# Kernel optimization log

Hardware: AMD Instinct MI355X
Metric: run time of the kernel (lower is better)

## Reference

```python
import jax, jax.numpy as jnp
import numpy as np

N = 100_000      # nodes (single heterogeneous node type)
E = 1_600_000    # edges per relation (avg in-degree ~16)
D = 128          # in_feats
H = 128          # rep_dim
R = 3            # relations


def setup_inputs() -> dict:
    key = jax.random.key(0)
    ks = jax.random.split(key, 1 + 6 * R)
    inp = {"x": jax.random.normal(ks[0], (N, D), jnp.float32)}
    for r in range(R):
        k = ks[1 + 6 * r: 1 + 6 * (r + 1)]
        inp[f"src{r}"] = jax.random.randint(k[0], (E,), 0, N)
        inp[f"dst{r}"] = jax.random.randint(k[1], (E,), 0, N)
        inp[f"w{r}"] = jax.random.uniform(k[2], (E,), jnp.float32)
        inp[f"Wself{r}"] = jax.random.normal(k[3], (D, H), jnp.float32) * 0.05
        inp[f"Wneigh{r}"] = jax.random.normal(k[4], (D, H), jnp.float32) * 0.05
        inp[f"b{r}"] = jax.random.normal(k[5], (H,), jnp.float32) * 0.05
    return inp


def _sage_mean(x, src, dst, w, Wself, Wneigh, b):
    """DGL SAGEConv, aggregator='mean', edge_weight=w, activation=ReLU.

    h_N[v] = (sum_{e:(u->v)} w_e * x[u]) / max(in_deg(v), 1)
    out    = relu(x @ Wself + h_N @ Wneigh + b)
    """
    msg = x[src] * w[:, None]                                   # [E, D] gather
    s = jax.ops.segment_sum(msg, dst, num_segments=N)           # [N, D] scatter-add
    deg = jax.ops.segment_sum(jnp.ones_like(w), dst, num_segments=N)  # [N]
    h_neigh = s / jnp.maximum(deg, 1.0)[:, None]                # mean; 0 for isolated nodes
    return jax.nn.relu(x @ Wself + h_neigh @ Wneigh + b)


def reference(x,
              src0, dst0, w0,
              src1, dst1, w1,
              src2, dst2, w2,
              Wself0, Wneigh0, b0,
              Wself1, Wneigh1, b1,
              Wself2, Wneigh2, b2):
    # HeteroGraphConv(aggregate='mean'): average the per-relation SAGEConv outputs.
    o0 = _sage_mean(x, src0, dst0, w0, Wself0, Wneigh0, b0)
    o1 = _sage_mean(x, src1, dst1, w1, Wself1, Wneigh1, b1)
    o2 = _sage_mean(x, src2, dst2, w2, Wself2, Wneigh2, b2)
    return (o0 + o1 + o2) / 3.0
```

## Files before the change

kernel.cpp:

```cpp
#include <hip/hip_runtime.h>
#include <hip/hip_bf16.h>
#include <cstdio>
#include <cstdint>
#include <cstddef>

#define NN 100000
#define EE 1600000
#define DD 128

#define BKT 196
#define RSHIFT 9
#define RANGE 512
#define CAP 9500
#define EPB 2048
#define ABLK ((EE + EPB - 1) / EPB)

typedef __attribute__((ext_vector_type(8))) short short8;
typedef __attribute__((ext_vector_type(4))) float floatx4;

__device__ __forceinline__ float bf2f(unsigned short u) {
    union { unsigned int u; float f; } c;
    c.u = ((unsigned int)u) << 16;
    return c.f;
}
__device__ __forceinline__ float hi2f(unsigned int p) {
    union { unsigned int u; float f; } c;
    c.u = p & 0xffff0000u;
    return c.f;
}
__device__ __forceinline__ float lo2f(unsigned int p) {
    union { unsigned int u; float f; } c;
    c.u = p << 16;
    return c.f;
}
__device__ __forceinline__ unsigned short f2bf(float f) {
    union { float f; unsigned int u; } c;
    c.f = f;
    unsigned int lsb = (c.u >> 16) & 1u;
    c.u += 0x7fffu + lsb;
    return (unsigned short)(c.u >> 16);
}

__global__ void detect_kernel(const void* x, const void* w, const void* Wm,
                              const void* b, int* flags) {
    __shared__ int ok_s;
    int bid = blockIdx.x, tid = threadIdx.x;
    if (tid == 0) ok_s = 0;
    __syncthreads();
    const unsigned short* p;
    int n;
    if (bid == 0)      { p = (const unsigned short*)x;  n = 1024; }
    else if (bid == 1) { p = (const unsigned short*)w;  n = 1024; }
    else if (bid == 2) { p = (const unsigned short*)Wm; n = 1024; }
    else               { p = (const unsigned short*)b;  n = 128;  }
    int ok = 0;
    for (int i = tid; i < n; i += blockDim.x) {
        unsigned short u = p[i];
        int e = (u >> 7) & 0xff;
        if (u == 0 || u == 0x8000 || (e >= 90 && e <= 127)) ok++;
    }
    atomicAdd(&ok_s, ok);
    __syncthreads();
    if (tid == 0) flags[bid] = (ok_s * 4 >= n * 3) ? 1 : 0;
}

__global__ void conv_x_kernel(const void* src, unsigned short* dst, int n4,
                              const int* flag) {
    if (*flag) return;
    int i = blockIdx.x * blockDim.x + threadIdx.x;
    if (i >= n4) return;
    float4 f = ((const float4*)src)[i];
    uint2 o;
    o.x = (unsigned int)f2bf(f.x) | ((unsigned int)f2bf(f.y) << 16);
    o.y = (unsigned int)f2bf(f.z) | ((unsigned int)f2bf(f.w) << 16);
    ((uint2*)dst)[i] = o;
}

__global__ void conv_bias_kernel(const void* b0, const void* b1,
                                 const void* b2, float* dst,
                                 const int* flag) {
    int r = blockIdx.x;
    const void* src = (r == 0) ? b0 : (r == 1) ? b1 : b2;
    int i = threadIdx.x;
    if (i >= DD) return;
    if (*flag) dst[r * DD + i] = bf2f(((const unsigned short*)src)[i]);
    else       dst[r * DD + i] = ((const float*)src)[i];
}

__global__ void wfrag_kernel(const void* W0s, const void* W0n, const void* W1s,
                             const void* W1n, const void* W2s, const void* W2n,
                             unsigned short* out, const int* flag) {
    int mat = blockIdx.x >> 3;
    const void* W = (mat == 0) ? W0s : (mat == 1) ? W0n : (mat == 2) ? W1s
                  : (mat == 3) ? W1n : (mat == 4) ? W2s : W2n;
    int gid = (blockIdx.x & 7) * 256 + threadIdx.x;
    int nt = gid >> 8;
    int kc = (gid >> 6) & 3;
    int lane = gid & 63;
    int n = nt * 16 + (lane & 15);
    int k0 = kc * 32 + (lane >> 4) * 8;
    unsigned short v[8];
    if (*flag) {
        const unsigned short* Ws = (const unsigned short*)W;
#pragma unroll
        for (int j = 0; j < 8; j++) v[j] = Ws[(k0 + j) * DD + n];
    } else {
        const float* Ws = (const float*)W;
#pragma unroll
        for (int j = 0; j < 8; j++) v[j] = f2bf(Ws[(k0 + j) * DD + n]);
    }
    *(short8*)(out + (size_t)mat * DD * DD + (size_t)gid * 8) = *(short8*)v;
}

__global__ void __launch_bounds__(256) countA_kernel(
    const int* __restrict__ d0, const int* __restrict__ d1,
    const int* __restrict__ d2, int* __restrict__ cnts) {
    __shared__ int hist[BKT];
    const int rel = blockIdx.x / ABLK;
    const int blk = blockIdx.x - rel * ABLK;
    const int* dstp = (rel == 0) ? d0 : (rel == 1) ? d1 : d2;
    int* cn = cnts + (size_t)rel * ABLK * BKT;
    const int tid = threadIdx.x;
    const int base = blk * EPB;
    for (int i = tid; i < BKT; i += 256) hist[i] = 0;
    __syncthreads();
#pragma unroll
    for (int k = 0; k < 8; k++) {
        int i = base + k * 256 + tid;
        if (i < EE) atomicAdd(&hist[dstp[i] >> RSHIFT], 1);
    }
    __syncthreads();
    for (int i = tid; i < BKT; i += 256)
        cn[(size_t)blk * BKT + i] = hist[i];
}

__global__ void __launch_bounds__(256) scanA_kernel(
    const int* __restrict__ cnts, int* __restrict__ bases,
    int* __restrict__ gcur) {
    __shared__ int s[256];
    const int rel = blockIdx.x / BKT;
    const int b = blockIdx.x - rel * BKT;
    const int* cn = cnts + (size_t)rel * ABLK * BKT;
    int* bs = bases + (size_t)rel * ABLK * BKT;
    const int tid = threadIdx.x;
    const int per = (ABLK + 255) / 256;
    int v[4];
    int sum = 0;
#pragma unroll
    for (int k = 0; k < 4; k++) {
        int idx = tid * per + k;
        v[k] = (idx < ABLK) ? cn[(size_t)idx * BKT + b] : 0;
        sum += v[k];
    }
    s[tid] = sum;
    __syncthreads();
    for (int o = 1; o < 256; o <<= 1) {
        int t = (tid >= o) ? s[tid - o] : 0;
        __syncthreads();
        s[tid] += t;
        __syncthreads();
    }
    int running = s[tid] - sum;
#pragma unroll
    for (int k = 0; k < 4; k++) {
        int idx = tid * per + k;
        if (idx < ABLK) bs[(size_t)idx * BKT + b] = running;
        running += v[k];
    }
    if (tid == 255) gcur[rel * BKT + b] = s[255];
}

__global__ void __launch_bounds__(256) placeA_kernel(
    const int* __restrict__ srcp, const int* __restrict__ dstp,
    const void* __restrict__ wp, const int* __restrict__ bases,
    int2* __restrict__ ebin, const int* __restrict__ wflag) {
    __shared__ int hist[BKT];
    __shared__ int off[BKT];
    __shared__ int cur[BKT];
    __shared__ int gbase[BKT];
    __shared__ int scan[256];
    __shared__ int2 sorted[EPB];
    __shared__ unsigned char slotb[EPB];
    const int tid = threadIdx.x;
    const int base = blockIdx.x * EPB;
    for (int i = tid; i < BKT; i += 256) hist[i] = 0;
    __syncthreads();
    int myd[8];
#pragma unroll
    for (int k = 0; k < 8; k++) {
        int i = base + k * 256 + tid;
        int d = (i < EE) ? dstp[i] : -1;
        myd[k] = d;
        if (d >= 0) atomicAdd(&hist[d >> RSHIFT], 1);
    }
    __syncthreads();
    int hv = (tid < BKT) ? hist[tid] : 0;
    scan[tid] = hv;
    __syncthreads();
    for (int o = 1; o < 256; o <<= 1) {
        int v = (tid >= o) ? scan[tid - o] : 0;
        __syncthreads();
        scan[tid] += v;
        __syncthreads();
    }
    if (tid < BKT) {
        off[tid] = scan[tid] - hv;
        cur[tid] = scan[tid] - hv;
        gbase[tid] = bases[(size_t)blockIdx.x * BKT + tid];
    }
    __syncthreads();
    const bool wbf = (*wflag != 0);
#pragma unroll
    for (int k = 0; k < 8; k++) {
        int d = myd[k];
        if (d < 0) continue;
        int i = base + k * 256 + tid;
        int b = d >> RSHIFT;
        int dloc = d - (b << RSHIFT);
        int s = srcp[i];
        float wv = wbf ? bf2f(((const unsigned short*)wp)[i])
                       : ((const float*)wp)[i];
        union { float f; int i; } c; c.f = wv;
        int pos = atomicAdd(&cur[b], 1);
        sorted[pos] = make_int2(s | (dloc << 17), c.i);
        slotb[pos] = (unsigned char)b;
    }
    __syncthreads();
    const int total = min(EPB, EE - base);
    for (int i = tid; i < total; i += 256) {
        int b = slotb[i];
        int g = gbase[b] + (i - off[b]);
        if (g < CAP) ebin[(size_t)b * CAP + g] = sorted[i];
    }
}

__global__ void __launch_bounds__(256) bucketsort_kernel(
    const int2* __restrict__ ebin, const int* __restrict__ gcur,
    int2* __restrict__ es2, int2* __restrict__ ptrv) {
    __shared__ int hc[RANGE];
    __shared__ int off[RANGE];
    __shared__ int scan[256];
    const int b = blockIdx.x, tid = threadIdx.x;
    const int base = b * CAP;
    const int cnt = min(gcur[b], CAP);
    for (int i = tid; i < RANGE; i += 256) hc[i] = 0;
    __syncthreads();
    for (int i = tid; i < cnt; i += 256) {
        int dl = ebin[base + i].x >> 17;
        atomicAdd(&hc[dl], 1);
    }
    __syncthreads();
    int a0 = hc[2 * tid], a1 = hc[2 * tid + 1];
    scan[tid] = a0 + a1;
    __syncthreads();
    for (int o = 1; o < 256; o <<= 1) {
        int v = (tid >= o) ? scan[tid - o] : 0;
        __syncthreads();
        scan[tid] += v;
        __syncthreads();
    }
    int ex = scan[tid] - (a0 + a1);
    off[2 * tid] = ex;
    off[2 * tid + 1] = ex + a0;
    ptrv[b * RANGE + 2 * tid]     = make_int2(base + ex, a0);
    ptrv[b * RANGE + 2 * tid + 1] = make_int2(base + ex + a0, a1);
    __syncthreads();
    hc[2 * tid] = off[2 * tid];
    hc[2 * tid + 1] = off[2 * tid + 1];
    __syncthreads();
    for (int i = tid; i < cnt; i += 256) {
        int2 rec = ebin[base + i];
        int dl = rec.x >> 17;
        int p = atomicAdd(&hc[dl], 1);
        es2[base + p] = make_int2(rec.x & 0x1FFFF, rec.y);
    }
}

__global__ void __launch_bounds__(256) aggregate_kernel(
    const int2* __restrict__ es2, const int2* __restrict__ ptrv,
    const unsigned short* __restrict__ xc, const void* __restrict__ xraw,
    const int* __restrict__ xflag, unsigned short* __restrict__ hout) {
    int gw = (blockIdx.x * blockDim.x + threadIdx.x) >> 6;
    int lane = threadIdx.x & 63;
    if (gw >= 3 * NN) return;
    int rel = gw / NN;
    int node = gw - rel * NN;
    const unsigned int* x32 = (*xflag) ? (const unsigned int*)xraw
                                       : (const unsigned int*)xc;
    const int2* es = es2 + (size_t)rel * BKT * CAP;
    int2 pc = ptrv[(size_t)rel * BKT * RANGE + node];
    int beg = pc.x, deg = pc.y, end = beg + deg;
    float a0 = 0.f, a1 = 0.f;
    int e = beg;
    for (; e + 16 <= end; e += 16) {
        unsigned int p[16];
        float cw[16];
#pragma unroll
        for (int k = 0; k < 16; k++) {
            int2 r = es[e + k];
            p[k] = x32[(size_t)r.x * 64 + lane];
            union { int i; float f; } c; c.i = r.y;
            cw[k] = c.f;
        }
#pragma unroll
        for (int k = 0; k < 16; k++) {
            a0 += cw[k] * lo2f(p[k]);
            a1 += cw[k] * hi2f(p[k]);
        }
    }
    for (; e + 4 <= end; e += 4) {
        int2 r0 = es[e], r1 = es[e + 1], r2 = es[e + 2], r3 = es[e + 3];
        unsigned int p0 = x32[(size_t)r0.x * 64 + lane];
        unsigned int p1 = x32[(size_t)r1.x * 64 + lane];
        unsigned int p2 = x32[(size_t)r2.x * 64 + lane];
        unsigned int p3 = x32[(size_t)r3.x * 64 + lane];
        union { int i; float f; } c0, c1, c2, c3;
        c0.i = r0.y; c1.i = r1.y; c2.i = r2.y; c3.i = r3.y;
        a0 += c0.f * lo2f(p0); a1 += c0.f * hi2f(p0);
        a0 += c1.f * lo2f(p1); a1 += c1.f * hi2f(p1);
        a0 += c2.f * lo2f(p2); a1 += c2.f * hi2f(p2);
        a0 += c3.f * lo2f(p3); a1 += c3.f * hi2f(p3);
    }
    for (; e < end; e++) {
        int2 r0 = es[e];
        unsigned int p0 = x32[(size_t)r0.x * 64 + lane];
        union { int i; float f; } c0; c0.i = r0.y;
        a0 += c0.f * lo2f(p0); a1 += c0.f * hi2f(p0);
    }
    float inv = 1.0f / (float)(deg > 1 ? deg : 1);
    unsigned int outv = ((unsigned int)f2bf(a1 * inv) << 16) | f2bf(a0 * inv);
    ((unsigned int*)hout)[(size_t)gw * 64 + lane] = outv;
}

__global__ void __launch_bounds__(256) output_kernel(
    const unsigned short* __restrict__ xc, const void* __restrict__ xraw,
    const unsigned short* __restrict__ h, const unsigned short* __restrict__ wf,
    const float* __restrict__ bc, void* out, const int* __restrict__ flag) {
    __shared__ unsigned short lds[DD * DD];
    const int tid = threadIdx.x;
    const int wv = tid >> 6, lane = tid & 63;
    const int tile = blockIdx.x * 4 + wv;
    const bool active = tile < (NN / 16);
    const int c = lane & 15, q = lane >> 4;
    const int nodeRow = tile * 16 + c;
    const int xbf = *flag;
    const unsigned short* xs = xbf ? (const unsigned short*)xraw : xc;

    short8 xfrag[4];
    if (active) {
#pragma unroll
        for (int kc = 0; kc < 4; kc++)
            xfrag[kc] = *(const short8*)(xs + (size_t)nodeRow * DD + kc * 32 +
                                         q * 8);
    }

    floatx4 outacc[8];
#pragma unroll
    for (int i = 0; i < 8; i++) outacc[i] = (floatx4){0.f, 0.f, 0.f, 0.f};

    for (int r = 0; r < 3; r++) {
        floatx4 acc[8];
#pragma unroll
        for (int i = 0; i < 8; i++) acc[i] = (floatx4){0.f, 0.f, 0.f, 0.f};
        for (int p = 0; p < 2; p++) {
            __syncthreads();
            {
                const int4* src = (const int4*)(wf + (size_t)(r * 2 + p) * DD * DD);
                int4* dst = (int4*)lds;
#pragma unroll
                for (int it = 0; it < 8; it++)
                    dst[tid + it * 256] = src[tid + it * 256];
            }
            __syncthreads();
            if (active) {
#pragma unroll
                for (int kc = 0; kc < 4; kc++) {
                    short8 afrag;
                    if (p == 0) {
                        afrag = xfrag[kc];
                    } else {
                        afrag = *(const short8*)(h + (size_t)r * NN * DD +
                                                 (size_t)nodeRow * DD +
                                                 kc * 32 + q * 8);
                    }
#pragma unroll
                    for (int nt = 0; nt < 8; nt++) {
                        short8 bfrag = *(const short8*)(
                            &lds[((nt * 4 + kc) * 64 + lane) * 8]);
                        acc[nt] = __builtin_amdgcn_mfma_f32_16x16x32_bf16(
                            afrag, bfrag, acc[nt], 0, 0, 0);
                    }
                }
            }
        }
        if (active) {
#pragma unroll
            for (int nt = 0; nt < 8; nt++) {
                float bv = bc[r * DD + nt * 16 + c];
#pragma unroll
                for (int i = 0; i < 4; i++) {
                    float v = acc[nt][i] + bv;
                    outacc[nt][i] += fmaxf(v, 0.f);
                }
            }
        }
    }
    if (active) {
        const float sc = 1.f / 3.f;
        if (xbf) {
            unsigned short* o = (unsigned short*)out;
#pragma unroll
            for (int nt = 0; nt < 8; nt++)
#pragma unroll
                for (int i = 0; i < 4; i++)
                    o[(size_t)(tile * 16 + q * 4 + i) * DD + nt * 16 + c] =
                        f2bf(outacc[nt][i] * sc);
        } else {
            float* o = (float*)out;
#pragma unroll
            for (int nt = 0; nt < 8; nt++)
#pragma unroll
                for (int i = 0; i < 4; i++)
                    o[(size_t)(tile * 16 + q * 4 + i) * DD + nt * 16 + c] =
                        outacc[nt][i] * sc;
        }
    }
}

extern "C" void kernel_launch(void* const* d_in, const int* in_sizes, int n_in,
                              void* d_out, int out_size, void* d_ws,
                              size_t ws_size, hipStream_t stream) {
    char* w = (char*)d_ws;
    size_t off = 0;
    auto alloc = [&](size_t bytes) {
        size_t o = off;
        off = (off + bytes + 255) & ~(size_t)255;
        return o;
    };
    size_t o_flags = alloc(4 * sizeof(int));
    size_t o_gcur  = alloc(3 * BKT * sizeof(int));
    size_t o_bc    = alloc(3 * DD * sizeof(float));
    size_t o_wf    = alloc(6 * DD * DD * sizeof(unsigned short));
    size_t o_xc    = alloc((size_t)NN * DD * sizeof(unsigned short));
    size_t o_cnts  = alloc((size_t)3 * ABLK * BKT * sizeof(int));
    size_t o_bases = alloc((size_t)3 * ABLK * BKT * sizeof(int));
    size_t o_ebin  = alloc((size_t)BKT * CAP * sizeof(int2));
    size_t o_es2   = alloc((size_t)3 * BKT * CAP * sizeof(int2));
    size_t o_ptrv  = alloc((size_t)3 * BKT * RANGE * sizeof(int2));
    size_t o_h     = alloc((size_t)3 * NN * DD * sizeof(unsigned short));
    if (ws_size < off) {
        fprintf(stderr, "kernel_launch: ws_size=%zu < needed=%zu\n", ws_size,
                off);
        return;
    }
    int* flags          = (int*)(w + o_flags);
    int* gcur           = (int*)(w + o_gcur);
    float* bc           = (float*)(w + o_bc);
    unsigned short* wf  = (unsigned short*)(w + o_wf);
    unsigned short* xc  = (unsigned short*)(w + o_xc);
    int* cnts           = (int*)(w + o_cnts);
    int* bases          = (int*)(w + o_bases);
    int2* ebin          = (int2*)(w + o_ebin);
    int2* es2           = (int2*)(w + o_es2);
    int2* ptrv          = (int2*)(w + o_ptrv);
    unsigned short* hh  = (unsigned short*)(w + o_h);

    const void* x_in = d_in[0];

    detect_kernel<<<4, 256, 0, stream>>>(x_in, d_in[3], d_in[4], d_in[6],
                                         flags);
    conv_x_kernel<<<(NN * DD / 4 + 255) / 256, 256, 0, stream>>>(
        x_in, xc, NN * DD / 4, flags + 0);
    wfrag_kernel<<<48, 256, 0, stream>>>(d_in[4], d_in[5], d_in[10], d_in[11],
                                         d_in[16], d_in[17], wf, flags + 2);
    conv_bias_kernel<<<3, 128, 0, stream>>>(d_in[6], d_in[12], d_in[18], bc,
                                            flags + 3);

    countA_kernel<<<3 * ABLK, 256, 0, stream>>>(
        (const int*)d_in[2], (const int*)d_in[8], (const int*)d_in[14], cnts);
    scanA_kernel<<<3 * BKT, 256, 0, stream>>>(cnts, bases, gcur);

    for (int r = 0; r < 3; r++) {
        int base = 1 + 6 * r;
        placeA_kernel<<<ABLK, 256, 0, stream>>>(
            (const int*)d_in[base + 0], (const int*)d_in[base + 1],
            d_in[base + 2], bases + (size_t)r * ABLK * BKT, ebin, flags + 1);
        bucketsort_kernel<<<BKT, 256, 0, stream>>>(
            ebin, gcur + r * BKT, es2 + (size_t)r * BKT * CAP,
            ptrv + (size_t)r * BKT * RANGE);
    }

    aggregate_kernel<<<(3 * NN + 3) / 4, 256, 0, stream>>>(
        es2, ptrv, xc, x_in, flags + 0, hh);

    const int NTILES = NN / 16;
    output_kernel<<<(NTILES + 3) / 4, 256, 0, stream>>>(xc, x_in, hh, wf, bc,
                                                        d_out, flags + 0);
}
```

Measured before the change: 554.8 us.

## Batch per-relation bucket sort launches and gather two edges per wave in aggregation

The placement and bucket-sort kernels now process all three relations in one launch each, using a separate bin buffer per relation when the workspace is large enough, and fall back to the per-relation loop otherwise. This removes launch serialisation and lets the GPU fill with three times as many blocks. The aggregation kernel now has each half-wave gather a different edge's row with 8-byte loads, combines the halves with a cross-lane shuffle, and makes edge bounds wave-uniform through readfirstlane. This doubles the number of rows fetched in flight per wave, at the cost of extra workspace and a reduction step.

```diff
diff --git a/kernel.cpp b/kernel.cpp
--- a/kernel.cpp
+++ b/kernel.cpp
@@ -32,6 +32,9 @@
     union { unsigned int u; float f; } c;
     c.u = p << 16;
     return c.f;
+}
+__device__ __forceinline__ float i2f(int i) {
+    union { int i; float f; } c; c.i = i; return c.f;
 }
 __device__ __forceinline__ unsigned short f2bf(float f) {
     union { float f; unsigned int u; } c;
@@ -119,7 +122,6 @@
     const int rel = blockIdx.x / ABLK;
     const int blk = blockIdx.x - rel * ABLK;
     const int* dstp = (rel == 0) ? d0 : (rel == 1) ? d1 : d2;
-    int* cn = cnts + (size_t)rel * ABLK * BKT;
     const int tid = threadIdx.x;
     const int base = blk * EPB;
     for (int i = tid; i < BKT; i += 256) hist[i] = 0;
@@ -131,7 +133,7 @@
     }
     __syncthreads();
     for (int i = tid; i < BKT; i += 256)
-        cn[(size_t)blk * BKT + i] = hist[i];
+        cnts[(size_t)blockIdx.x * BKT + i] = hist[i];
 }
 
 __global__ void __launch_bounds__(256) scanA_kernel(
@@ -171,8 +173,11 @@
 }
 
 __global__ void __launch_bounds__(256) placeA_kernel(
-    const int* __restrict__ srcp, const int* __restrict__ dstp,
-    const void* __restrict__ wp, const int* __restrict__ bases,
+    const int* __restrict__ s0, const int* __restrict__ d0,
+    const void* __restrict__ w0, const int* __restrict__ s1,
+    const int* __restrict__ d1, const void* __restrict__ w1,
+    const int* __restrict__ s2, const int* __restrict__ d2,
+    const void* __restrict__ w2, const int* __restrict__ bases,
     int2* __restrict__ ebin, const int* __restrict__ wflag) {
     __shared__ int hist[BKT];
     __shared__ int off[BKT];
@@ -181,8 +186,14 @@
     __shared__ int scan[256];
     __shared__ int2 sorted[EPB];
     __shared__ unsigned char slotb[EPB];
+    const int rel = blockIdx.x / ABLK;
+    const int blk = blockIdx.x - rel * ABLK;
+    const int* srcp = (rel == 0) ? s0 : (rel == 1) ? s1 : s2;
+    const int* dstp = (rel == 0) ? d0 : (rel == 1) ? d1 : d2;
+    const void* wp  = (rel == 0) ? w0 : (rel == 1) ? w1 : w2;
+    int2* eb = ebin + (size_t)rel * BKT * CAP;
     const int tid = threadIdx.x;
-    const int base = blockIdx.x * EPB;
+    const int base = blk * EPB;
     for (int i = tid; i < BKT; i += 256) hist[i] = 0;
     __syncthreads();
     int myd[8];
@@ -230,7 +241,7 @@
     for (int i = tid; i < total; i += 256) {
         int b = slotb[i];
         int g = gbase[b] + (i - off[b]);
-        if (g < CAP) ebin[(size_t)b * CAP + g] = sorted[i];
+        if (g < CAP) eb[(size_t)b * CAP + g] = sorted[i];
     }
 }
 
@@ -240,13 +251,18 @@
     __shared__ int hc[RANGE];
     __shared__ int off[RANGE];
     __shared__ int scan[256];
-    const int b = blockIdx.x, tid = threadIdx.x;
+    const int rel = blockIdx.x / BKT;
+    const int b = blockIdx.x - rel * BKT;
+    const int2* eb = ebin + (size_t)rel * BKT * CAP;
+    int2* es = es2 + (size_t)rel * BKT * CAP;
+    int2* pv = ptrv + (size_t)rel * BKT * RANGE;
+    const int tid = threadIdx.x;
     const int base = b * CAP;
-    const int cnt = min(gcur[b], CAP);
+    const int cnt = min(gcur[rel * BKT + b], CAP);
     for (int i = tid; i < RANGE; i += 256) hc[i] = 0;
     __syncthreads();
     for (int i = tid; i < cnt; i += 256) {
-        int dl = ebin[base + i].x >> 17;
+        int dl = eb[base + i].x >> 17;
         atomicAdd(&hc[dl], 1);
     }
     __syncthreads();
@@ -262,17 +278,17 @@
     int ex = scan[tid] - (a0 + a1);
     off[2 * tid] = ex;
     off[2 * tid + 1] = ex + a0;
-    ptrv[b * RANGE + 2 * tid]     = make_int2(base + ex, a0);
-    ptrv[b * RANGE + 2 * tid + 1] = make_int2(base + ex + a0, a1);
+    pv[b * RANGE + 2 * tid]     = make_int2(base + ex, a0);
+    pv[b * RANGE + 2 * tid + 1] = make_int2(base + ex + a0, a1);
     __syncthreads();
     hc[2 * tid] = off[2 * tid];
     hc[2 * tid + 1] = off[2 * tid + 1];
     __syncthreads();
     for (int i = tid; i < cnt; i += 256) {
-        int2 rec = ebin[base + i];
+        int2 rec = eb[base + i];
         int dl = rec.x >> 17;
         int p = atomicAdd(&hc[dl], 1);
-        es2[base + p] = make_int2(rec.x & 0x1FFFF, rec.y);
+        es[base + p] = make_int2(rec.x & 0x1FFFF, rec.y);
     }
 }
 
@@ -280,56 +296,63 @@
     const int2* __restrict__ es2, const int2* __restrict__ ptrv,
     const unsigned short* __restrict__ xc, const void* __restrict__ xraw,
     const int* __restrict__ xflag, unsigned short* __restrict__ hout) {
-    int gw = (blockIdx.x * blockDim.x + threadIdx.x) >> 6;
+    int gw = __builtin_amdgcn_readfirstlane(
+        (blockIdx.x * blockDim.x + threadIdx.x) >> 6);
     int lane = threadIdx.x & 63;
     if (gw >= 3 * NN) return;
     int rel = gw / NN;
     int node = gw - rel * NN;
-    const unsigned int* x32 = (*xflag) ? (const unsigned int*)xraw
-                                       : (const unsigned int*)xc;
+    const uint2* x64 = (*xflag) ? (const uint2*)xraw : (const uint2*)xc;
     const int2* es = es2 + (size_t)rel * BKT * CAP;
     int2 pc = ptrv[(size_t)rel * BKT * RANGE + node];
-    int beg = pc.x, deg = pc.y, end = beg + deg;
-    float a0 = 0.f, a1 = 0.f;
+    int beg = __builtin_amdgcn_readfirstlane(pc.x);
+    int deg = __builtin_amdgcn_readfirstlane(pc.y);
+    int end = beg + deg;
+    const int half = lane >> 5, l5 = lane & 31;
+    float a0 = 0.f, a1 = 0.f, a2 = 0.f, a3 = 0.f;
     int e = beg;
     for (; e + 16 <= end; e += 16) {
-        unsigned int p[16];
-        float cw[16];
-#pragma unroll
-        for (int k = 0; k < 16; k++) {
-            int2 r = es[e + k];
-            p[k] = x32[(size_t)r.x * 64 + lane];
-            union { int i; float f; } c; c.i = r.y;
-            cw[k] = c.f;
+        int2 rec[16];
+#pragma unroll
+        for (int k = 0; k < 16; k++) rec[k] = es[e + k];
+#pragma unroll
+        for (int k = 0; k < 8; k++) {
+            int2 rA = rec[2 * k], rB = rec[2 * k + 1];
+            int src = half ? rB.x : rA.x;
+            float wv = i2f(half ? rB.y : rA.y);
+            uint2 px = x64[(size_t)src * 32 + l5];
+            a0 += wv * lo2f(px.x); a1 += wv * hi2f(px.x);
+            a2 += wv * lo2f(px.y); a3 += wv * hi2f(px.y);
         }
-#pragma unroll
-        for (int k = 0; k < 16; k++) {
-            a0 += cw[k] * lo2f(p[k]);
-            a1 += cw[k] * hi2f(p[k]);
-        }
-    }
-    for (; e + 4 <= end; e += 4) {
-        int2 r0 = es[e], r1 = es[e + 1], r2 = es[e + 2], r3 = es[e + 3];
-        unsigned int p0 = x32[(size_t)r0.x * 64 + lane];
-        unsigned int p1 = x32[(size_t)r1.x * 64 + lane];
-        unsigned int p2 = x32[(size_t)r2.x * 64 + lane];
-        unsigned int p3 = x32[(size_t)r3.x * 64 + lane];
-        union { int i; float f; } c0, c1, c2, c3;
-        c0.i = r0.y; c1.i = r1.y; c2.i = r2.y; c3.i = r3.y;
-        a0 += c0.f * lo2f(p0); a1 += c0.f * hi2f(p0);
-        a0 += c1.f * lo2f(p1); a1 += c1.f * hi2f(p1);
-        a0 += c2.f * lo2f(p2); a1 += c2.f * hi2f(p2);
-        a0 += c3.f * lo2f(p3); a1 += c3.f * hi2f(p3);
-    }
-    for (; e < end; e++) {
-        int2 r0 = es[e];
-        unsigned int p0 = x32[(size_t)r0.x * 64 + lane];
-        union { int i; float f; } c0; c0.i = r0.y;
-        a0 += c0.f * lo2f(p0); a1 += c0.f * hi2f(p0);
-    }
+    }
+    for (; e + 2 <= end; e += 2) {
+        int2 rA = es[e], rB = es[e + 1];
+        int src = half ? rB.x : rA.x;
+        float wv = i2f(half ? rB.y : rA.y);
+        uint2 px = x64[(size_t)src * 32 + l5];
+        a0 += wv * lo2f(px.x); a1 += wv * hi2f(px.x);
+        a2 += wv * lo2f(px.y); a3 += wv * hi2f(px.y);
+    }
+    if (e < end) {
+        int2 rA = es[e];
+        float wv = half ? 0.f : i2f(rA.y);
+        uint2 px = x64[(size_t)rA.x * 32 + l5];
+        a0 += wv * lo2f(px.x); a1 += wv * hi2f(px.x);
+        a2 += wv * lo2f(px.y); a3 += wv * hi2f(px.y);
+    }
+    a0 += __shfl_xor(a0, 32);
+    a1 += __shfl_xor(a1, 32);
+    a2 += __shfl_xor(a2, 32);
+    a3 += __shfl_xor(a3, 32);
     float inv = 1.0f / (float)(deg > 1 ? deg : 1);
-    unsigned int outv = ((unsigned int)f2bf(a1 * inv) << 16) | f2bf(a0 * inv);
-    ((unsigned int*)hout)[(size_t)gw * 64 + lane] = outv;
+    if (half == 0) {
+        uint2 o;
+        o.x = (unsigned int)f2bf(a0 * inv) |
+              ((unsigned int)f2bf(a1 * inv) << 16);
+        o.y = (unsigned int)f2bf(a2 * inv) |
+              ((unsigned int)f2bf(a3 * inv) << 16);
+        ((uint2*)hout)[(size_t)gw * 32 + l5] = o;
+    }
 }
 
 __global__ void __launch_bounds__(256) output_kernel(
@@ -444,15 +467,20 @@
     size_t o_xc    = alloc((size_t)NN * DD * sizeof(unsigned short));
     size_t o_cnts  = alloc((size_t)3 * ABLK * BKT * sizeof(int));
     size_t o_bases = alloc((size_t)3 * ABLK * BKT * sizeof(int));
-    size_t o_ebin  = alloc((size_t)BKT * CAP * sizeof(int2));
     size_t o_es2   = alloc((size_t)3 * BKT * CAP * sizeof(int2));
     size_t o_ptrv  = alloc((size_t)3 * BKT * RANGE * sizeof(int2));
     size_t o_h     = alloc((size_t)3 * NN * DD * sizeof(unsigned short));
-    if (ws_size < off) {
+    size_t o_ebin  = off;
+    size_t ebin_bytes = (size_t)BKT * CAP * sizeof(int2);
+    size_t need1 = o_ebin + ebin_bytes;
+    size_t need3 = o_ebin + 3 * ebin_bytes;
+    if (ws_size < need1) {
         fprintf(stderr, "kernel_launch: ws_size=%zu < needed=%zu\n", ws_size,
-                off);
+                need1);
         return;
     }
+    const bool batched = (ws_size >= need3);
+
     int* flags          = (int*)(w + o_flags);
     int* gcur           = (int*)(w + o_gcur);
     float* bc           = (float*)(w + o_bc);
@@ -460,10 +488,10 @@
     unsigned short* xc  = (unsigned short*)(w + o_xc);
     int* cnts           = (int*)(w + o_cnts);
     int* bases          = (int*)(w + o_bases);
-    int2* ebin          = (int2*)(w + o_ebin);
     int2* es2           = (int2*)(w + o_es2);
     int2* ptrv          = (int2*)(w + o_ptrv);
     unsigned short* hh  = (unsigned short*)(w + o_h);
+    int2* ebin          = (int2*)(w + o_ebin);
 
     const void* x_in = d_in[0];
 
@@ -480,14 +508,26 @@
         (const int*)d_in[2], (const int*)d_in[8], (const int*)d_in[14], cnts);
     scanA_kernel<<<3 * BKT, 256, 0, stream>>>(cnts, bases, gcur);
 
-    for (int r = 0; r < 3; r++) {
-        int base = 1 + 6 * r;
-        placeA_kernel<<<ABLK, 256, 0, stream>>>(
-            (const int*)d_in[base + 0], (const int*)d_in[base + 1],
-            d_in[base + 2], bases + (size_t)r * ABLK * BKT, ebin, flags + 1);
-        bucketsort_kernel<<<BKT, 256, 0, stream>>>(
-            ebin, gcur + r * BKT, es2 + (size_t)r * BKT * CAP,
-            ptrv + (size_t)r * BKT * RANGE);
+    if (batched) {
+        placeA_kernel<<<3 * ABLK, 256, 0, stream>>>(
+            (const int*)d_in[1], (const int*)d_in[2], d_in[3],
+            (const int*)d_in[7], (const int*)d_in[8], d_in[9],
+            (const int*)d_in[13], (const int*)d_in[14], d_in[15], bases, ebin,
+            flags + 1);
+        bucketsort_kernel<<<3 * BKT, 256, 0, stream>>>(ebin, gcur, es2, ptrv);
+    } else {
+        for (int r = 0; r < 3; r++) {
+            int base = 1 + 6 * r;
+            const int* sp = (const int*)d_in[base + 0];
+            const int* dp = (const int*)d_in[base + 1];
+            const void* wp = d_in[base + 2];
+            placeA_kernel<<<ABLK, 256, 0, stream>>>(
+                sp, dp, wp, sp, dp, wp, sp, dp, wp,
+                bases + (size_t)r * ABLK * BKT, ebin, flags + 1);
+            bucketsort_kernel<<<BKT, 256, 0, stream>>>(
+                ebin, gcur + r * BKT, es2 + (size_t)r * BKT * CAP,
+                ptrv + (size_t)r * BKT * RANGE);
+        }
     }
 
     aggregate_kernel<<<(3 * NN + 3) / 4, 256, 0, stream>>>(
```

Measured after the change: 516.2 us. 1.07x faster.
